# Optimization experiments

Hardware: AMD Instinct MI355X
Metric: run time of the kernel (lower is better)

Reference implementation:

```python
import jax, jax.numpy as jnp
import numpy as np

N, D, F, E, K = 8192, 1024, 4096, 8, 2


def setup_inputs() -> dict:
    key = jax.random.key(0)
    ks = jax.random.split(key, 4)
    x = jax.random.normal(ks[0], (N, D), dtype=jnp.float32)
    Wg = jax.random.normal(ks[1], (D, E), dtype=jnp.float32) * 0.02
    W1 = jax.random.normal(ks[2], (E, D, F), dtype=jnp.float32) * 0.02
    b1 = jnp.zeros((E, F), dtype=jnp.float32)
    W2 = jax.random.normal(ks[3], (E, F, D), dtype=jnp.float32) * 0.02
    b2 = jnp.zeros((E, D), dtype=jnp.float32)
    return {"x": x, "Wg": Wg, "W1": W1, "b1": b1, "W2": W2, "b2": b2}


def reference(x, Wg, W1, b1, W2, b2):
    # Top-k softmax gate (TopKGate): pick K experts per token, renormalize.
    logits = x @ Wg                                        # [N, E]
    probs = jax.nn.softmax(logits, axis=-1)
    gate_vals, expert_idx = jax.lax.top_k(probs, K)        # [N, K]
    gate_w = gate_vals / jnp.sum(gate_vals, axis=-1, keepdims=True)

    # Expert FFN (dispatch/combine math): the torch code sorts tokens by expert
    # id, all-to-alls them to the owning rank, applies the local Expert MLP,
    # and combines back weighted by gate_w. The jit-friendly equivalent is to
    # compute every expert's MLP for all tokens and gather the selected rows.
    h = jax.nn.relu(jnp.einsum('nd,edf->enf', x, W1) + b1[:, None, :])  # [E, N, F]
    o = jnp.einsum('enf,efd->end', h, W2) + b2[:, None, :]               # [E, N, D]

    tok = jnp.arange(x.shape[0])
    sel = o[expert_idx, tok[:, None]]                      # [N, K, D]
    y = jnp.sum(gate_w[..., None] * sel, axis=1)           # [N, D]
    return y
```

## Files before the change

kernel.cpp:

```cpp
#include <hip/hip_runtime.h>

#define N_TOK 8192
#define DIM   1024
#define FFN   4096
#define NEXP  8
#define TOPK  2
#define NENT  (N_TOK * TOPK)
#define MAXM  20

using short8   = __attribute__((ext_vector_type(8))) short;
using ushort8v = __attribute__((ext_vector_type(8))) unsigned short;
using floatx4  = __attribute__((ext_vector_type(4))) float;

__device__ __forceinline__ unsigned short f2bf(float f) {
    union { float f; unsigned u; } v; v.f = f;
    unsigned r = v.u + 0x7fffu + ((v.u >> 16) & 1u);
    return (unsigned short)(r >> 16);
}

#define GLOAD_LDS16(gptr, lptr) __builtin_amdgcn_global_load_lds( \
    (__attribute__((address_space(1))) void*)(void*)(gptr),       \
    (__attribute__((address_space(3))) void*)(lptr), 16, 0, 0)


__device__ __forceinline__ void transpose_tile(const float* __restrict__ inp,
                                               unsigned short* __restrict__ outp,
                                               int R, int C, int r0, int c0,
                                               float* __restrict__ tile) {
    int t = threadIdx.x;
    int p = t & 7;
    int trow = t >> 3;
    int w = t >> 6;
#pragma unroll
    for (int i = 0; i < 8; i++) {
        int r = i * 32 + trow;
        float4 v = *(const float4*)&inp[(size_t)(r0 + r) * C + c0 + p * 4];
        int cc = p ^ ((4 * i + w) & 7);
        *(float4*)&tile[r * 32 + cc * 4] = v;
    }
    __syncthreads();
    int c = t >> 3;
    int cbase = ((c >> 2) ^ p) * 4 + (c & 3);
    unsigned short* orow = outp + (size_t)(c0 + c) * R + r0;
#pragma unroll
    for (int j = 0; j < 4; j++) {
        int rb = j * 64 + p * 8;
        ushort8v us;
#pragma unroll
        for (int k = 0; k < 8; k++)
            us[k] = f2bf(tile[(rb + k) * 32 + cbase]);
        *(ushort8v*)&orow[rb] = us;
    }
}


__global__ __launch_bounds__(256) void prep_kernel(
    const float* __restrict__ W1, unsigned short* __restrict__ w1t,
    const float* __restrict__ x, const float* __restrict__ wg,
    unsigned short* __restrict__ xb,
    int* __restrict__ topk_e, float* __restrict__ topk_w,
    int* __restrict__ counts)
{
    __shared__ float tile[8192];
    int bid = blockIdx.x;
    if (bid < 4096) {
        int rt = bid & 3;
        int ct = (bid >> 2) & 127;
        int e  = bid >> 9;
        transpose_tile(W1 + (size_t)e * DIM * FFN, w1t + (size_t)e * DIM * FFN,
                       DIM, FFN, rt * 256, ct * 32, tile);
        return;
    }

    int tid = threadIdx.x;
    int wave = tid >> 6, lane = tid & 63;
    int t = (bid - 4096) * 4 + wave;
    const float* xr = x + (size_t)t * DIM;
    unsigned short* xbr = xb + (size_t)t * DIM;
    float acc[NEXP];
#pragma unroll
    for (int e = 0; e < NEXP; e++) acc[e] = 0.f;
    for (int it = 0; it < DIM / 256; it++) {
        int d = it * 256 + lane * 4;
        float4 xv = *(const float4*)&xr[d];
        ushort4 ub;
        ub.x = f2bf(xv.x); ub.y = f2bf(xv.y); ub.z = f2bf(xv.z); ub.w = f2bf(xv.w);
        *(ushort4*)&xbr[d] = ub;
        const float* wp = wg + (size_t)d * NEXP;
#pragma unroll
        for (int j = 0; j < 4; j++) {
            float xj = (j == 0) ? xv.x : (j == 1) ? xv.y : (j == 2) ? xv.z : xv.w;
            const float4* wr = (const float4*)(wp + j * NEXP);
            float4 w0 = wr[0], w1 = wr[1];
            acc[0] += xj * w0.x; acc[1] += xj * w0.y; acc[2] += xj * w0.z; acc[3] += xj * w0.w;
            acc[4] += xj * w1.x; acc[5] += xj * w1.y; acc[6] += xj * w1.z; acc[7] += xj * w1.w;
        }
    }
#pragma unroll
    for (int e = 0; e < NEXP; e++) {
#pragma unroll
        for (int off = 32; off > 0; off >>= 1) acc[e] += __shfl_xor(acc[e], off);
    }
    if (lane == 0) {
        int e1 = 0; float l1 = acc[0];
        for (int e = 1; e < NEXP; e++) if (acc[e] > l1) { l1 = acc[e]; e1 = e; }
        int e2 = -1; float l2 = -3.4e38f;
        for (int e = 0; e < NEXP; e++) if (e != e1 && acc[e] > l2) { l2 = acc[e]; e2 = e; }
        float w1v = 1.f / (1.f + expf(l2 - l1));
        topk_e[t * 2]     = e1;  topk_e[t * 2 + 1] = e2;
        topk_w[t * 2]     = w1v; topk_w[t * 2 + 1] = 1.f - w1v;
        atomicAdd(&counts[e1], 1);
        atomicAdd(&counts[e2], 1);
    }
}


__global__ __launch_bounds__(256) void scatter_kernel(const int* __restrict__ topk_e,
                                                      const float* __restrict__ topk_w,
                                                      const int* __restrict__ counts,
                                                      int* __restrict__ offs,
                                                      int* __restrict__ cursors,
                                                      int* __restrict__ entry_token,
                                                      float* __restrict__ entry_w) {
    int off_[NEXP]; int s = 0;
#pragma unroll
    for (int e = 0; e < NEXP; e++) { off_[e] = s; s += counts[e]; }
    if (blockIdx.x == 0 && threadIdx.x == 0) {
#pragma unroll
        for (int e = 0; e < NEXP; e++) offs[e] = off_[e];
        offs[NEXP] = s;
    }
    int t = blockIdx.x * 256 + threadIdx.x;
#pragma unroll
    for (int k = 0; k < TOPK; k++) {
        int e = topk_e[t * 2 + k];
        int pos = off_[e] + atomicAdd(&cursors[e], 1);
        entry_token[pos] = t;
        entry_w[pos] = topk_w[t * 2 + k];
    }
}


union __align__(16) G1Smem {
    struct { unsigned short As[2][4096]; unsigned short Bs[2][4096]; int toks[128]; } g;
    float tile[8192];
};

__global__ __launch_bounds__(256, 3) void gemm1_kernel(
    const unsigned short* __restrict__ xb,
    const unsigned short* __restrict__ w1t,
    const float* __restrict__ b1,
    const int* __restrict__ offs,
    const int* __restrict__ entry_token,
    unsigned short* __restrict__ h,
    const float* __restrict__ W2,
    unsigned short* __restrict__ w2t)
{
    __shared__ G1Smem sm;
    int bid0 = blockIdx.x;
    if (bid0 < 4096) {
        int rt = bid0 & 15;
        int ct = (bid0 >> 4) & 31;
        int e  = bid0 >> 9;
        transpose_tile(W2 + (size_t)e * DIM * FFN, w2t + (size_t)e * DIM * FFN,
                       FFN, DIM, rt * 256, ct * 32, sm.tile);
        return;
    }

    int bid   = bid0 - 4096;
    int xcd   = bid & 7;
    int inner = bid >> 3;
    int gq    = inner / MAXM;
    int mt    = inner - gq * MAXM;
    int g     = gq * 8 + xcd;
    int e     = g >> 5;
    int nt    = g & 31;
    int base = offs[e];
    int cnt  = offs[e + 1] - base;
    int m0   = mt * 128;
    if (m0 >= cnt) return;
    int f0   = nt * 128;

    auto& As   = sm.g.As;
    auto& Bs   = sm.g.Bs;
    auto& toks = sm.g.toks;

    int tid = threadIdx.x;
    if (tid < 128) {
        int r = m0 + tid;
        toks[tid] = entry_token[base + (r < cnt ? r : 0)];
    }
    __syncthreads();

    int wave = tid >> 6, lane = tid & 63;
    int wm = (wave >> 1) * 64, wn = (wave & 1) * 64;

    int lr = lane >> 2, sl = lane & 3;
    int g0 = (sl ^ ((lr >> 1) & 3)) * 8;
    const unsigned short* aG[2];
    const unsigned short* bG[2];
    int ldsOff[2];
#pragma unroll
    for (int c = 0; c < 2; c++) {
        int row = wave * 32 + c * 16 + lr;
        aG[c] = xb + (size_t)toks[row] * DIM + g0;
        bG[c] = w1t + ((size_t)e * FFN + f0 + row) * DIM + g0;
        ldsOff[c] = (wave * 32 + c * 16) * 32;
    }

    floatx4 acc[4][4];
#pragma unroll
    for (int i = 0; i < 4; i++)
#pragma unroll
        for (int j = 0; j < 4; j++) acc[i][j] = (floatx4)0.f;

    int quad = lane >> 4, rm = lane & 15;
    int slf  = (quad ^ ((rm >> 1) & 3)) * 8;
    int arow = (wm + rm) * 32;
    int brow = (wn + rm) * 32;

#pragma unroll
    for (int c = 0; c < 2; c++) {
        GLOAD_LDS16(aG[c], &As[0][ldsOff[c]]);
        GLOAD_LDS16(bG[c], &Bs[0][ldsOff[c]]);
        aG[c] += 32; bG[c] += 32;
    }

    int cur = 0;
    for (int kk = 0; kk < DIM / 32; kk++) {
        __syncthreads();
        short8 af[4], bfr[4];
#pragma unroll
        for (int mi = 0; mi < 4; mi++) af[mi] = *(const short8*)&As[cur][arow + mi * 512 + slf];
#pragma unroll
        for (int ni = 0; ni < 4; ni++) bfr[ni] = *(const short8*)&Bs[cur][brow + ni * 512 + slf];
        if (kk + 1 < DIM / 32) {
            int nxt = cur ^ 1;
#pragma unroll
            for (int c = 0; c < 2; c++) {
                GLOAD_LDS16(aG[c], &As[nxt][ldsOff[c]]);
                GLOAD_LDS16(bG[c], &Bs[nxt][ldsOff[c]]);
                aG[c] += 32; bG[c] += 32;
            }
        }
#pragma unroll
        for (int mi = 0; mi < 4; mi++)
#pragma unroll
            for (int ni = 0; ni < 4; ni++)
                acc[mi][ni] = __builtin_amdgcn_mfma_f32_16x16x32_bf16(af[mi], bfr[ni], acc[mi][ni], 0, 0, 0);
        cur ^= 1;
    }

#pragma unroll
    for (int mi = 0; mi < 4; mi++) {
        int mbase = wm + mi * 16 + quad * 4;
#pragma unroll
        for (int ni = 0; ni < 4; ni++) {
            int f = f0 + wn + ni * 16 + rm;
            float bias = b1[e * FFN + f];
            floatx4 v = acc[mi][ni];
#pragma unroll
            for (int r = 0; r < 4; r++) {
                int row = m0 + mbase + r;
                if (row < cnt) {
                    float t = v[r] + bias;
                    t = t > 0.f ? t : 0.f;
                    h[(size_t)(base + row) * FFN + f] = f2bf(t);
                }
            }
        }
    }
}


__global__ __launch_bounds__(256, 3) void gemm2_kernel(
    const unsigned short* __restrict__ h,
    const unsigned short* __restrict__ w2t,
    const float* __restrict__ b2,
    const int* __restrict__ offs,
    const int* __restrict__ entry_token,
    const float* __restrict__ entry_w,
    float* __restrict__ y)
{
    int bid  = blockIdx.x;
    int e    = bid & 7;
    int grp  = bid % (8 * MAXM);
    int mt   = grp >> 3;
    int nt   = bid / (8 * MAXM);
    int base = offs[e];
    int cnt  = offs[e + 1] - base;
    int m0   = mt * 128;
    if (m0 >= cnt) return;
    int n0   = nt * 128;

    __shared__ unsigned short As[2][128 * 32];
    __shared__ unsigned short Bs[2][128 * 32];

    int tid = threadIdx.x;
    int wave = tid >> 6, lane = tid & 63;
    int wm = (wave >> 1) * 64, wn = (wave & 1) * 64;

    int lr = lane >> 2, sl = lane & 3;
    int g0 = (sl ^ ((lr >> 1) & 3)) * 8;
    const unsigned short* aG[2];
    const unsigned short* bG[2];
    int ldsOff[2];
#pragma unroll
    for (int c = 0; c < 2; c++) {
        int row = wave * 32 + c * 16 + lr;
        aG[c] = h + (size_t)(base + m0 + row) * FFN + g0;
        bG[c] = w2t + ((size_t)e * DIM + n0 + row) * FFN + g0;
        ldsOff[c] = (wave * 32 + c * 16) * 32;
    }

    floatx4 acc[4][4];
#pragma unroll
    for (int i = 0; i < 4; i++)
#pragma unroll
        for (int j = 0; j < 4; j++) acc[i][j] = (floatx4)0.f;

    int quad = lane >> 4, rm = lane & 15;
    int slf  = (quad ^ ((rm >> 1) & 3)) * 8;
    int arow = (wm + rm) * 32;
    int brow = (wn + rm) * 32;

#pragma unroll
    for (int c = 0; c < 2; c++) {
        GLOAD_LDS16(aG[c], &As[0][ldsOff[c]]);
        GLOAD_LDS16(bG[c], &Bs[0][ldsOff[c]]);
        aG[c] += 32; bG[c] += 32;
    }

    int cur = 0;
    for (int kk = 0; kk < FFN / 32; kk++) {
        __syncthreads();
        short8 af[4], bfr[4];
#pragma unroll
        for (int mi = 0; mi < 4; mi++) af[mi] = *(const short8*)&As[cur][arow + mi * 512 + slf];
#pragma unroll
        for (int ni = 0; ni < 4; ni++) bfr[ni] = *(const short8*)&Bs[cur][brow + ni * 512 + slf];
        if (kk + 1 < FFN / 32) {
            int nxt = cur ^ 1;
#pragma unroll
            for (int c = 0; c < 2; c++) {
                GLOAD_LDS16(aG[c], &As[nxt][ldsOff[c]]);
                GLOAD_LDS16(bG[c], &Bs[nxt][ldsOff[c]]);
                aG[c] += 32; bG[c] += 32;
            }
        }
#pragma unroll
        for (int mi = 0; mi < 4; mi++)
#pragma unroll
            for (int ni = 0; ni < 4; ni++)
                acc[mi][ni] = __builtin_amdgcn_mfma_f32_16x16x32_bf16(af[mi], bfr[ni], acc[mi][ni], 0, 0, 0);
        cur ^= 1;
    }

    float bs[4];
#pragma unroll
    for (int ni = 0; ni < 4; ni++) bs[ni] = b2[e * DIM + n0 + wn + ni * 16 + rm];
#pragma unroll
    for (int mi = 0; mi < 4; mi++) {
        int mbase = wm + mi * 16 + quad * 4;
#pragma unroll
        for (int r = 0; r < 4; r++) {
            int row = m0 + mbase + r;
            if (row < cnt) {
                int tok = entry_token[base + row];
                float w = entry_w[base + row];
                float* yr = y + (size_t)tok * DIM;
#pragma unroll
                for (int ni = 0; ni < 4; ni++) {
                    int n = n0 + wn + ni * 16 + rm;
                    atomicAdd(&yr[n], w * (acc[mi][ni][r] + bs[ni]));
                }
            }
        }
    }
}


extern "C" void kernel_launch(void* const* d_in, const int* in_sizes, int n_in,
                              void* d_out, int out_size, void* d_ws, size_t ws_size,
                              hipStream_t stream) {
    const float* x  = (const float*)d_in[0];
    const float* Wg = (const float*)d_in[1];
    const float* W1 = (const float*)d_in[2];
    const float* b1 = (const float*)d_in[3];
    const float* W2 = (const float*)d_in[4];
    const float* b2 = (const float*)d_in[5];
    float* y = (float*)d_out;

    char* p = (char*)d_ws;
    unsigned short* xb  = (unsigned short*)p; p += (size_t)N_TOK * DIM * 2;
    unsigned short* w1t = (unsigned short*)p; p += (size_t)NEXP * DIM * FFN * 2;
    unsigned short* w2t = (unsigned short*)p; p += (size_t)NEXP * DIM * FFN * 2;
    unsigned short* h   = (unsigned short*)p; p += (size_t)(NENT + 128) * FFN * 2;
    int*   topk_e      = (int*)p;   p += (size_t)N_TOK * TOPK * 4;
    float* topk_w      = (float*)p; p += (size_t)N_TOK * TOPK * 4;
    int*   entry_token = (int*)p;   p += (size_t)NENT * 4;
    float* entry_w     = (float*)p; p += (size_t)NENT * 4;
    int*   counts      = (int*)p;   p += NEXP * 4;
    int*   cursors     = (int*)p;   p += NEXP * 4;
    int*   offs        = (int*)p;   p += (NEXP + 1) * 4;

    hipMemsetAsync(counts, 0, NEXP * 4 * 2, stream);
    hipMemsetAsync(y, 0, (size_t)N_TOK * DIM * 4, stream);

    prep_kernel<<<4096 + N_TOK / 4, 256, 0, stream>>>(W1, w1t, x, Wg, xb,
                                                      topk_e, topk_w, counts);
    scatter_kernel<<<N_TOK / 256, 256, 0, stream>>>(topk_e, topk_w, counts, offs,
                                                    cursors, entry_token, entry_w);
    gemm1_kernel<<<4096 + NEXP * MAXM * (FFN / 128), 256, 0, stream>>>(
        xb, w1t, b1, offs, entry_token, h, W2, w2t);
    gemm2_kernel<<<NEXP * MAXM * (DIM / 128), 256, 0, stream>>>(h, w2t, b2, offs,
                                                                entry_token, entry_w, y);
}
```

Baseline: 992.5 us.

## Fuse MoE pipeline into one persistent cooperative kernel with atomic work queues

Replaces four kernel launches and two memsets with one cooperative persistent kernel. Its phases (weight transposes plus gating, scatter plus zeroing of y, expert GEMM1, expert GEMM2) are separated by grid-wide syncs. GEMM tiles are handed out through per-XCD atomic work queues, so blocks whose tiles are empty move on instead of idling. This removes launch gaps and load imbalance between phases, at the cost of grid.sync barriers, occupancy fixed at launch, and extra atomics for each tile fetch.

```diff
diff --git a/kernel.cpp b/kernel.cpp
--- a/kernel.cpp
+++ b/kernel.cpp
@@ -1,4 +1,7 @@
 #include <hip/hip_runtime.h>
+#include <hip/hip_cooperative_groups.h>
+
+namespace cg = cooperative_groups;
 
 #define N_TOK 8192
 #define DIM   1024
@@ -22,11 +25,25 @@
     (__attribute__((address_space(1))) void*)(void*)(gptr),       \
     (__attribute__((address_space(3))) void*)(lptr), 16, 0, 0)
 
+struct MoeArgs {
+    const float* x; const float* Wg; const float* W1; const float* b1;
+    const float* W2; const float* b2;
+    unsigned short* xb; unsigned short* w1t; unsigned short* w2t; unsigned short* h;
+    int* topk_e; float* topk_w; int* entry_token; float* entry_w;
+    int* counters;
+    float* y;
+};
+
+union __align__(16) Smem {
+    struct { unsigned short As[2][4096]; unsigned short Bs[2][4096]; int toks[128]; } g;
+    float tile[8192];
+};
+
 
 __device__ __forceinline__ void transpose_tile(const float* __restrict__ inp,
                                                unsigned short* __restrict__ outp,
                                                int R, int C, int r0, int c0,
-                                               float* __restrict__ tile) {
+                                               float* tile) {
     int t = threadIdx.x;
     int p = t & 7;
     int trow = t >> 3;
@@ -54,29 +71,12 @@
 }
 
 
-__global__ __launch_bounds__(256) void prep_kernel(
-    const float* __restrict__ W1, unsigned short* __restrict__ w1t,
-    const float* __restrict__ x, const float* __restrict__ wg,
-    unsigned short* __restrict__ xb,
-    int* __restrict__ topk_e, float* __restrict__ topk_w,
-    int* __restrict__ counts)
-{
-    __shared__ float tile[8192];
-    int bid = blockIdx.x;
-    if (bid < 4096) {
-        int rt = bid & 3;
-        int ct = (bid >> 2) & 127;
-        int e  = bid >> 9;
-        transpose_tile(W1 + (size_t)e * DIM * FFN, w1t + (size_t)e * DIM * FFN,
-                       DIM, FFN, rt * 256, ct * 32, tile);
-        return;
-    }
-
+__device__ void gating_job(const MoeArgs& a, int gj) {
     int tid = threadIdx.x;
     int wave = tid >> 6, lane = tid & 63;
-    int t = (bid - 4096) * 4 + wave;
-    const float* xr = x + (size_t)t * DIM;
-    unsigned short* xbr = xb + (size_t)t * DIM;
+    int t = gj * 4 + wave;
+    const float* xr = a.x + (size_t)t * DIM;
+    unsigned short* xbr = a.xb + (size_t)t * DIM;
     float acc[NEXP];
 #pragma unroll
     for (int e = 0; e < NEXP; e++) acc[e] = 0.f;
@@ -86,7 +86,7 @@
         ushort4 ub;
         ub.x = f2bf(xv.x); ub.y = f2bf(xv.y); ub.z = f2bf(xv.z); ub.w = f2bf(xv.w);
         *(ushort4*)&xbr[d] = ub;
-        const float* wp = wg + (size_t)d * NEXP;
+        const float* wp = a.Wg + (size_t)d * NEXP;
 #pragma unroll
         for (int j = 0; j < 4; j++) {
             float xj = (j == 0) ? xv.x : (j == 1) ? xv.y : (j == 2) ? xv.z : xv.w;
@@ -107,67 +107,15 @@
         int e2 = -1; float l2 = -3.4e38f;
         for (int e = 0; e < NEXP; e++) if (e != e1 && acc[e] > l2) { l2 = acc[e]; e2 = e; }
         float w1v = 1.f / (1.f + expf(l2 - l1));
-        topk_e[t * 2]     = e1;  topk_e[t * 2 + 1] = e2;
-        topk_w[t * 2]     = w1v; topk_w[t * 2 + 1] = 1.f - w1v;
-        atomicAdd(&counts[e1], 1);
-        atomicAdd(&counts[e2], 1);
-    }
-}
-
-
-__global__ __launch_bounds__(256) void scatter_kernel(const int* __restrict__ topk_e,
-                                                      const float* __restrict__ topk_w,
-                                                      const int* __restrict__ counts,
-                                                      int* __restrict__ offs,
-                                                      int* __restrict__ cursors,
-                                                      int* __restrict__ entry_token,
-                                                      float* __restrict__ entry_w) {
-    int off_[NEXP]; int s = 0;
-#pragma unroll
-    for (int e = 0; e < NEXP; e++) { off_[e] = s; s += counts[e]; }
-    if (blockIdx.x == 0 && threadIdx.x == 0) {
-#pragma unroll
-        for (int e = 0; e < NEXP; e++) offs[e] = off_[e];
-        offs[NEXP] = s;
-    }
-    int t = blockIdx.x * 256 + threadIdx.x;
-#pragma unroll
-    for (int k = 0; k < TOPK; k++) {
-        int e = topk_e[t * 2 + k];
-        int pos = off_[e] + atomicAdd(&cursors[e], 1);
-        entry_token[pos] = t;
-        entry_w[pos] = topk_w[t * 2 + k];
-    }
-}
-
-
-union __align__(16) G1Smem {
-    struct { unsigned short As[2][4096]; unsigned short Bs[2][4096]; int toks[128]; } g;
-    float tile[8192];
-};
-
-__global__ __launch_bounds__(256, 3) void gemm1_kernel(
-    const unsigned short* __restrict__ xb,
-    const unsigned short* __restrict__ w1t,
-    const float* __restrict__ b1,
-    const int* __restrict__ offs,
-    const int* __restrict__ entry_token,
-    unsigned short* __restrict__ h,
-    const float* __restrict__ W2,
-    unsigned short* __restrict__ w2t)
-{
-    __shared__ G1Smem sm;
-    int bid0 = blockIdx.x;
-    if (bid0 < 4096) {
-        int rt = bid0 & 15;
-        int ct = (bid0 >> 4) & 31;
-        int e  = bid0 >> 9;
-        transpose_tile(W2 + (size_t)e * DIM * FFN, w2t + (size_t)e * DIM * FFN,
-                       FFN, DIM, rt * 256, ct * 32, sm.tile);
-        return;
-    }
-
-    int bid   = bid0 - 4096;
+        a.topk_e[t * 2]     = e1;  a.topk_e[t * 2 + 1] = e2;
+        a.topk_w[t * 2]     = w1v; a.topk_w[t * 2 + 1] = 1.f - w1v;
+        atomicAdd(&a.counters[e1], 1);
+        atomicAdd(&a.counters[e2], 1);
+    }
+}
+
+
+__device__ void gemm1_job(const MoeArgs& a, Smem& sm, int bid) {
     int xcd   = bid & 7;
     int inner = bid >> 3;
     int gq    = inner / MAXM;
@@ -175,11 +123,12 @@
     int g     = gq * 8 + xcd;
     int e     = g >> 5;
     int nt    = g & 31;
-    int base = offs[e];
-    int cnt  = offs[e + 1] - base;
-    int m0   = mt * 128;
+    int base = 0;
+    for (int i = 0; i < e; i++) base += a.counters[i];
+    int cnt = a.counters[e];
+    int m0  = mt * 128;
     if (m0 >= cnt) return;
-    int f0   = nt * 128;
+    int f0  = nt * 128;
 
     auto& As   = sm.g.As;
     auto& Bs   = sm.g.Bs;
@@ -188,7 +137,7 @@
     int tid = threadIdx.x;
     if (tid < 128) {
         int r = m0 + tid;
-        toks[tid] = entry_token[base + (r < cnt ? r : 0)];
+        toks[tid] = a.entry_token[base + (r < cnt ? r : 0)];
     }
     __syncthreads();
 
@@ -203,8 +152,8 @@
 #pragma unroll
     for (int c = 0; c < 2; c++) {
         int row = wave * 32 + c * 16 + lr;
-        aG[c] = xb + (size_t)toks[row] * DIM + g0;
-        bG[c] = w1t + ((size_t)e * FFN + f0 + row) * DIM + g0;
+        aG[c] = a.xb + (size_t)toks[row] * DIM + g0;
+        bG[c] = a.w1t + ((size_t)e * FFN + f0 + row) * DIM + g0;
         ldsOff[c] = (wave * 32 + c * 16) * 32;
     }
 
@@ -257,7 +206,7 @@
 #pragma unroll
         for (int ni = 0; ni < 4; ni++) {
             int f = f0 + wn + ni * 16 + rm;
-            float bias = b1[e * FFN + f];
+            float bias = a.b1[e * FFN + f];
             floatx4 v = acc[mi][ni];
 #pragma unroll
             for (int r = 0; r < 4; r++) {
@@ -265,7 +214,7 @@
                 if (row < cnt) {
                     float t = v[r] + bias;
                     t = t > 0.f ? t : 0.f;
-                    h[(size_t)(base + row) * FFN + f] = f2bf(t);
+                    a.h[(size_t)(base + row) * FFN + f] = f2bf(t);
                 }
             }
         }
@@ -273,28 +222,20 @@
 }
 
 
-__global__ __launch_bounds__(256, 3) void gemm2_kernel(
-    const unsigned short* __restrict__ h,
-    const unsigned short* __restrict__ w2t,
-    const float* __restrict__ b2,
-    const int* __restrict__ offs,
-    const int* __restrict__ entry_token,
-    const float* __restrict__ entry_w,
-    float* __restrict__ y)
-{
-    int bid  = blockIdx.x;
+__device__ void gemm2_job(const MoeArgs& a, Smem& sm, int bid) {
     int e    = bid & 7;
     int grp  = bid % (8 * MAXM);
     int mt   = grp >> 3;
     int nt   = bid / (8 * MAXM);
-    int base = offs[e];
-    int cnt  = offs[e + 1] - base;
-    int m0   = mt * 128;
+    int base = 0;
+    for (int i = 0; i < e; i++) base += a.counters[i];
+    int cnt = a.counters[e];
+    int m0  = mt * 128;
     if (m0 >= cnt) return;
-    int n0   = nt * 128;
-
-    __shared__ unsigned short As[2][128 * 32];
-    __shared__ unsigned short Bs[2][128 * 32];
+    int n0  = nt * 128;
+
+    auto& As = sm.g.As;
+    auto& Bs = sm.g.Bs;
 
     int tid = threadIdx.x;
     int wave = tid >> 6, lane = tid & 63;
@@ -308,8 +249,8 @@
 #pragma unroll
     for (int c = 0; c < 2; c++) {
         int row = wave * 32 + c * 16 + lr;
-        aG[c] = h + (size_t)(base + m0 + row) * FFN + g0;
-        bG[c] = w2t + ((size_t)e * DIM + n0 + row) * FFN + g0;
+        aG[c] = a.h + (size_t)(base + m0 + row) * FFN + g0;
+        bG[c] = a.w2t + ((size_t)e * DIM + n0 + row) * FFN + g0;
         ldsOff[c] = (wave * 32 + c * 16) * 32;
     }
 
@@ -358,7 +299,7 @@
 
     float bs[4];
 #pragma unroll
-    for (int ni = 0; ni < 4; ni++) bs[ni] = b2[e * DIM + n0 + wn + ni * 16 + rm];
+    for (int ni = 0; ni < 4; ni++) bs[ni] = a.b2[e * DIM + n0 + wn + ni * 16 + rm];
 #pragma unroll
     for (int mi = 0; mi < 4; mi++) {
         int mbase = wm + mi * 16 + quad * 4;
@@ -366,9 +307,9 @@
         for (int r = 0; r < 4; r++) {
             int row = m0 + mbase + r;
             if (row < cnt) {
-                int tok = entry_token[base + row];
-                float w = entry_w[base + row];
-                float* yr = y + (size_t)tok * DIM;
+                int tok = a.entry_token[base + row];
+                float w = a.entry_w[base + row];
+                float* yr = a.y + (size_t)tok * DIM;
 #pragma unroll
                 for (int ni = 0; ni < 4; ni++) {
                     int n = n0 + wn + ni * 16 + rm;
@@ -376,6 +317,79 @@
                 }
             }
         }
+    }
+}
+
+
+__global__ __launch_bounds__(256, 3) void moe_kernel(MoeArgs a) {
+    __shared__ Smem sm;
+    __shared__ int nextJob;
+    cg::grid_group grid = cg::this_grid();
+    int nb = gridDim.x, bx = blockIdx.x, tid = threadIdx.x;
+    int* qC = a.counters + 16;
+    int* qD = a.counters + 24;
+
+    for (int vb = bx; vb < 10240; vb += nb) {
+        if (vb < 4096) {
+            int rt = vb & 3, ct = (vb >> 2) & 127, e = vb >> 9;
+            transpose_tile(a.W1 + (size_t)e * DIM * FFN, a.w1t + (size_t)e * DIM * FFN,
+                           DIM, FFN, rt * 256, ct * 32, sm.tile);
+            __syncthreads();
+        } else if (vb < 8192) {
+            int tb = vb - 4096;
+            int rt = tb & 15, ct = (tb >> 4) & 31, e = tb >> 9;
+            transpose_tile(a.W2 + (size_t)e * DIM * FFN, a.w2t + (size_t)e * DIM * FFN,
+                           FFN, DIM, rt * 256, ct * 32, sm.tile);
+            __syncthreads();
+        } else {
+            gating_job(a, vb - 8192);
+        }
+    }
+    grid.sync();
+
+    for (int vb = bx; vb < 544; vb += nb) {
+        if (vb < 32) {
+            int off_[NEXP]; int s = 0;
+#pragma unroll
+            for (int e = 0; e < NEXP; e++) { off_[e] = s; s += a.counters[e]; }
+            int* cursors = a.counters + 8;
+            int t = vb * 256 + tid;
+#pragma unroll
+            for (int k = 0; k < TOPK; k++) {
+                int e = a.topk_e[t * 2 + k];
+                int pos = off_[e] + atomicAdd(&cursors[e], 1);
+                a.entry_token[pos] = t;
+                a.entry_w[pos] = a.topk_w[t * 2 + k];
+            }
+        } else {
+            float4 z = make_float4(0.f, 0.f, 0.f, 0.f);
+            float4* yp = (float4*)a.y;
+            size_t b0 = (size_t)(vb - 32) * 256 + tid;
+#pragma unroll
+            for (int i = 0; i < 16; i++)
+                yp[b0 + (size_t)i * 512 * 256] = z;
+        }
+    }
+    grid.sync();
+
+    int myq = bx & 7;
+    for (;;) {
+        if (tid == 0) nextJob = atomicAdd(&qC[myq], 1);
+        __syncthreads();
+        int inner = nextJob;
+        if (inner >= 640) break;
+        gemm1_job(a, sm, inner * 8 + myq);
+        __syncthreads();
+    }
+    grid.sync();
+
+    for (;;) {
+        if (tid == 0) nextJob = atomicAdd(&qD[myq], 1);
+        __syncthreads();
+        int inner = nextJob;
+        if (inner >= 160) break;
+        gemm2_job(a, sm, inner * 8 + myq);
+        __syncthreads();
     }
 }
 
@@ -400,19 +414,26 @@
     float* topk_w      = (float*)p; p += (size_t)N_TOK * TOPK * 4;
     int*   entry_token = (int*)p;   p += (size_t)NENT * 4;
     float* entry_w     = (float*)p; p += (size_t)NENT * 4;
-    int*   counts      = (int*)p;   p += NEXP * 4;
-    int*   cursors     = (int*)p;   p += NEXP * 4;
-    int*   offs        = (int*)p;   p += (NEXP + 1) * 4;
-
-    hipMemsetAsync(counts, 0, NEXP * 4 * 2, stream);
-    hipMemsetAsync(y, 0, (size_t)N_TOK * DIM * 4, stream);
-
-    prep_kernel<<<4096 + N_TOK / 4, 256, 0, stream>>>(W1, w1t, x, Wg, xb,
-                                                      topk_e, topk_w, counts);
-    scatter_kernel<<<N_TOK / 256, 256, 0, stream>>>(topk_e, topk_w, counts, offs,
-                                                    cursors, entry_token, entry_w);
-    gemm1_kernel<<<4096 + NEXP * MAXM * (FFN / 128), 256, 0, stream>>>(
-        xb, w1t, b1, offs, entry_token, h, W2, w2t);
-    gemm2_kernel<<<NEXP * MAXM * (DIM / 128), 256, 0, stream>>>(h, w2t, b2, offs,
-                                                                entry_token, entry_w, y);
-}
+    int*   counters    = (int*)p;   p += 32 * 4;
+
+    hipMemsetAsync(counters, 0, 32 * 4, stream);
+
+    static int nblk = 0;
+    if (nblk == 0) {
+        int mb = 0;
+        hipOccupancyMaxActiveBlocksPerMultiprocessor(&mb, moe_kernel, 256, 0);
+        if (mb < 1) mb = 1;
+        if (mb > 3) mb = 3;
+        nblk = 256 * mb;
+    }
+
+    MoeArgs args;
+    args.x = x; args.Wg = Wg; args.W1 = W1; args.b1 = b1; args.W2 = W2; args.b2 = b2;
+    args.xb = xb; args.w1t = w1t; args.w2t = w2t; args.h = h;
+    args.topk_e = topk_e; args.topk_w = topk_w;
+    args.entry_token = entry_token; args.entry_w = entry_w;
+    args.counters = counters; args.y = y;
+
+    void* kp[] = { &args };
+    hipLaunchCooperativeKernel(moe_kernel, dim3(nblk), dim3(256), kp, 0, stream);
+}
```

New measurement: 1.538 ms. +55.0%, slower.
